# Kernel optimization log

Hardware: AMD Instinct MI355X
Metric: run time of the kernel (lower is better)

Reference implementation:

```python
import jax, jax.numpy as jnp
import numpy as np

B_, S_, IN_, D_, N_, K_ = 16, 4096, 64, 256, 16, 32


def _ln(x, g, b):
    m = jnp.mean(x, axis=-1, keepdims=True)
    v = jnp.var(x, axis=-1, keepdims=True)
    return (x - m) * jax.lax.rsqrt(v + 1e-5) * g + b


def setup_inputs() -> dict:
    key = jax.random.key(0)
    ks = jax.random.split(key, 24)
    s = 0.02
    d = dict(
        x=jax.random.normal(ks[0], (B_, S_, IN_), jnp.float32),
        W_in=jax.random.normal(ks[1], (IN_, D_)) * s, b_in=jnp.zeros((D_,)),
        ln1_g=jnp.ones((D_,)), ln1_b=jnp.zeros((D_,)),
        conv_w=jax.random.normal(ks[2], (D_, 1, 3)) * s, conv_b=jnp.zeros((D_,)),
        Wd=jax.random.normal(ks[3], (D_, D_)) * s, bd=jnp.zeros((D_,)),
        WB=jax.random.normal(ks[4], (D_, N_)) * s, bB=jnp.zeros((N_,)),
        WC=jax.random.normal(ks[5], (D_, N_)) * s, bC=jnp.zeros((N_,)),
        A=-jax.random.uniform(ks[6], (D_, N_)),
        Wg=jax.random.normal(ks[7], (D_, D_)) * s, bg=jnp.zeros((D_,)),
        filt_re=jax.random.normal(ks[8], (K_, D_)) * s,
        filt_im=jax.random.normal(ks[9], (K_, D_)) * s,
        alpha=jnp.ones((D_,)), beta=jnp.ones((D_,)),
        lnc_g=jnp.ones((D_,)), lnc_b=jnp.zeros((D_,)),
        W1=jax.random.normal(ks[10], (D_, D_ // 2)) * s, b1=jnp.zeros((D_ // 2,)),
        W2=jax.random.normal(ks[11], (D_ // 2, 2)) * s, b2=jnp.zeros((2,)),
    )
    return d


def reference(x, W_in, b_in, ln1_g, ln1_b, conv_w, conv_b, Wd, bd, WB, bB, WC, bC,
              A, Wg, bg, filt_re, filt_im, alpha, beta, lnc_g, lnc_b, W1, b1, W2, b2):
    xp = x @ W_in + b_in                                   # [B,S,D]

    # ---- TemporalBlock ----
    xn = _ln(xp, ln1_g, ln1_b)
    xc = jax.lax.conv_general_dilated(
        jnp.swapaxes(xn, 1, 2), conv_w, (1,), [(1, 1)],
        feature_group_count=D_, dimension_numbers=('NCH', 'OIH', 'NCH'))
    xc = jnp.swapaxes(xc + conv_b[:, None], 1, 2)          # [B,S,D]
    u = jax.nn.silu(xc)

    delta = jax.nn.softplus(u @ Wd + bd)                   # [B,S,D]
    Bm = u @ WB + bB                                       # [B,S,N]
    Cm = u @ WC + bC                                       # [B,S,N]

    def step(h, inp):
        u_t, d_t, B_t, C_t = inp                           # [B,D],[B,D],[B,N],[B,N]
        h = (1.0 + d_t[:, :, None] * A) * h + d_t[:, :, None] * B_t[:, None, :] * u_t[:, :, None]
        y_t = jnp.sum(C_t[:, None, :] * h, axis=-1)        # [B,D]
        return h, y_t

    h0 = jnp.zeros((u.shape[0], D_, N_), u.dtype)
    xs = tuple(jnp.swapaxes(a, 0, 1) for a in (u, delta, Bm, Cm))
    _, ys = jax.lax.scan(step, h0, xs)
    x_ssm = jnp.swapaxes(ys, 0, 1)                         # [B,S,D]
    g = jax.nn.silu(xn @ Wg + bg)
    x_t = xp + x_ssm * g

    # ---- SpectralBlock ----
    Xf = jnp.fft.rfft(xp, axis=1)                          # [B,F,D] complex
    mag = jnp.abs(Xf)
    _, idx = jax.lax.top_k(jnp.swapaxes(mag, 1, 2), K_)    # [B,D,K]
    idx = jnp.swapaxes(idx, 1, 2)                          # [B,K,D]
    sel = jnp.take_along_axis(Xf, idx, axis=1)             # [B,K,D]
    filt = filt_re + 1j * filt_im                          # [K,D]
    filtered = sel * filt[None]
    bi = jnp.arange(Xf.shape[0])[:, None, None]
    di = jnp.arange(D_)[None, None, :]
    Xfil = jnp.zeros_like(Xf).at[bi, idx, di].set(filtered)
    x_f = jnp.fft.irfft(Xfil, n=xp.shape[1], axis=1)       # [B,S,D]

    # ---- Fusion + classifier (eval: dropout = identity) ----
    z = alpha * x_t + beta * x_f
    zp = jnp.mean(z, axis=1)                               # [B,D]
    hcls = jax.nn.relu(_ln(zp, lnc_g, lnc_b) @ W1 + b1)
    return hcls @ W2 + b2                                  # [B,2]
```

## Files before the change

kernel.cpp:

```cpp
#include <hip/hip_runtime.h>
#include <hip/hip_bf16.h>
#include <math.h>

#define BB 16
#define SS 4096
#define IN 64
#define DD 256
#define NN 16
#define KK 32
#define CH 64
#define LCH 64
#define BS (BB*SS)

typedef __attribute__((ext_vector_type(4))) float f32x4;
typedef __attribute__((ext_vector_type(8))) short bf16x8;

__device__ __forceinline__ float bf2f(unsigned short u){
  return __uint_as_float(((unsigned int)u)<<16);
}
__device__ __forceinline__ unsigned short f2bf(float f){
  unsigned int u = __float_as_uint(f);
  return (unsigned short)((u + 0x7fffu + ((u>>16)&1u)) >> 16);
}
__device__ __forceinline__ float fast_softplus(float v){
  float e = __expf(-fabsf(v));
  return fmaxf(v, 0.f) + __logf(1.f + e);
}
__device__ __forceinline__ float fast_silu(float v){
  return v * __builtin_amdgcn_rcpf(1.f + __expf(-v));
}
__device__ __forceinline__ void* swz(void* base, int row, int byteoff){
  return (void*)((char*)base + (row<<9) + (byteoff ^ ((row&7)<<4)));
}
#define SW(i) ((i) ^ (((i)>>4)&15))
__device__ __forceinline__ int rev4(int k){
  return ((k&3)<<10) | (((k>>2)&3)<<8) | (((k>>4)&3)<<6)
       | (((k>>6)&3)<<4) | (((k>>8)&3)<<2) | ((k>>10)&3);
}

__global__ void k_prep(const float* Wd, const float* Wg, const float* WB, const float* WC,
                       const float* W_in, const float* bBv, const float* bCv,
                       unsigned short* WdF, unsigned short* WgF, unsigned short* WinF,
                       float* bbc, float2* tw){
  int id = blockIdx.x*256 + threadIdx.x;
  if (id < 73728){
    int jn = id >> 12; int rem = id & 4095;
    int kc = rem >> 9; int l8 = (rem >> 3) & 63; int e = id & 7;
    int lr = l8 & 15, lh = l8 >> 4;
    int k = kc*32 + lh*8 + e;
    float v;
    if (jn < 16){ int n = jn*16 + lr; v = Wd[k*256+n]; }
    else { int c = (jn-16)*16 + lr; v = (c<16) ? WB[k*16+c] : WC[k*16+(c-16)]; }
    WdF[id] = f2bf(v);
  }
  else if (id < 139264){
    int o = id - 73728;
    int jn = o >> 12; int rem = o & 4095;
    int kc = rem >> 9; int l8 = (rem >> 3) & 63; int e = o & 7;
    int lr = l8 & 15, lh = l8 >> 4;
    int k = kc*32 + lh*8 + e;
    WgF[o] = f2bf(Wg[k*256 + jn*16 + lr]);
  }
  else if (id < 155648){
    int o = id - 139264;
    int jn = o >> 10; int rem = o & 1023;
    int kc = rem >> 9; int l8 = (rem >> 3) & 63; int e = o & 7;
    int lr = l8 & 15, lh = l8 >> 4;
    int k = kc*32 + lh*8 + e;
    WinF[o] = f2bf(W_in[k*256 + jn*16 + lr]);
  }
  else if (id < 157696){ int k = id-155648;
    double a = -6.283185307179586476925287 * (double)k / 4096.0;
    tw[k] = make_float2((float)cos(a), (float)sin(a)); }
  else if (id < 157728){ int j = id-157696; bbc[j] = (j<16)? bBv[j] : bCv[j-16]; }
}

__global__ __launch_bounds__(256) void k_front(const float* x, const unsigned short* WinF, const float* b_in,
      const float* ln1_g, const float* ln1_b, const float* conv_w, const float* conv_b,
      float2* xpz, unsigned short* xn16, unsigned short* u16){
  __shared__ unsigned short xb[32*64];
  __shared__ float xs[20][260];
  int tid = threadIdx.x;
  int b = blockIdx.y; int t0 = blockIdx.x*16;
  {
    int row = tid>>3, slot = tid&7;
    int t = t0 - 1 + row;
    unsigned short h[8];
    if (row < 18 && t >= 0 && t < SS){
      const float* src = &x[((size_t)b*SS + t)*IN + slot*8];
      float4 v0 = *(const float4*)src;
      float4 v1 = *(const float4*)(src+4);
      h[0]=f2bf(v0.x); h[1]=f2bf(v0.y); h[2]=f2bf(v0.z); h[3]=f2bf(v0.w);
      h[4]=f2bf(v1.x); h[5]=f2bf(v1.y); h[6]=f2bf(v1.z); h[7]=f2bf(v1.w);
    } else {
      #pragma unroll
      for (int i=0;i<8;i++) h[i]=0;
    }
    *(uint4*)&xb[row*64 + ((slot ^ (row&7))<<3)] = *(uint4*)h;
  }
  __syncthreads();
  int wv = tid>>6, lane = tid&63, lr = lane&15, lh = lane>>4;
  {
    bf16x8 af[2][2];
    #pragma unroll
    for (int rf=0;rf<2;rf++)
      #pragma unroll
      for (int kc=0;kc<2;kc++){
        int row = rf*16 + lr;
        int slot = (kc*4 + lh) ^ (row&7);
        af[rf][kc] = *(const bf16x8*)&xb[row*64 + slot*8];
      }
    f32x4 acc[2][4];
    #pragma unroll
    for (int rf=0;rf<2;rf++)
      #pragma unroll
      for (int jj=0;jj<4;jj++){ acc[rf][jj][0]=0.f; acc[rf][jj][1]=0.f; acc[rf][jj][2]=0.f; acc[rf][jj][3]=0.f; }
    #pragma unroll
    for (int jj=0;jj<4;jj++){
      int jn = wv*4 + jj;
      const bf16x8* bp = (const bf16x8*)(WinF + (size_t)jn*1024 + (size_t)lane*8);
      bf16x8 b0 = bp[0];
      bf16x8 b1 = bp[64];
      #pragma unroll
      for (int rf=0;rf<2;rf++){
        acc[rf][jj] = __builtin_amdgcn_mfma_f32_16x16x32_bf16(af[rf][0], b0, acc[rf][jj], 0,0,0);
        acc[rf][jj] = __builtin_amdgcn_mfma_f32_16x16x32_bf16(af[rf][1], b1, acc[rf][jj], 0,0,0);
      }
    }
    #pragma unroll
    for (int jj=0;jj<4;jj++){
      int col = (wv*4+jj)*16 + lr;
      float bs = b_in[col];
      #pragma unroll
      for (int rf=0;rf<2;rf++){
        #pragma unroll
        for (int i=0;i<4;i++){
          int row = rf*16 + lh*4 + i;
          if (row < 18) xs[row][col] = acc[rf][jj][i] + bs;
        }
      }
    }
  }
  __syncthreads();
  {
    int sl = tid&15, p0 = tid>>4;
    float2* dst = xpz + (size_t)b*128*SS + t0 + sl;
    #pragma unroll
    for (int pass=0; pass<8; pass++){
      int p = p0 + 16*pass;
      float2 v = *(const float2*)&xs[1+sl][2*p];
      dst[(size_t)p*SS] = v;
    }
  }
  __syncthreads();
  float4 lg4 = *(const float4*)&ln1_g[lane*4];
  float4 lb4 = *(const float4*)&ln1_b[lane*4];
  for (int r=wv; r<18; r+=4){
    int t = t0 - 1 + r;
    bool valid = (t>=0) && (t<SS);
    float4 v = *(const float4*)&xs[r][lane*4];
    float s1 = v.x+v.y+v.z+v.w;
    float s2 = v.x*v.x+v.y*v.y+v.z*v.z+v.w*v.w;
    #pragma unroll
    for (int off=32; off; off>>=1){ s1 += __shfl_xor(s1,off); s2 += __shfl_xor(s2,off); }
    float mean = s1*(1.f/256.f);
    float var  = s2*(1.f/256.f) - mean*mean;
    float rstd = rsqrtf(var + 1e-5f);
    float o0 = valid ? ((v.x-mean)*rstd*lg4.x + lb4.x) : 0.f;
    float o1 = valid ? ((v.y-mean)*rstd*lg4.y + lb4.y) : 0.f;
    float o2 = valid ? ((v.z-mean)*rstd*lg4.z + lb4.z) : 0.f;
    float o3 = valid ? ((v.w-mean)*rstd*lg4.w + lb4.w) : 0.f;
    *(float4*)&xs[r][lane*4] = make_float4(o0,o1,o2,o3);
    if (r>=1 && r<=16){
      ushort4 st;
      st.x=f2bf(o0); st.y=f2bf(o1); st.z=f2bf(o2); st.w=f2bf(o3);
      *(ushort4*)&xn16[((size_t)b*SS + t)*DD + lane*4] = st;
    }
  }
  __syncthreads();
  int d = tid;
  float w0=conv_w[d*3], w1=conv_w[d*3+1], w2=conv_w[d*3+2], cb=conv_b[d];
  #pragma unroll 4
  for (int rr=0; rr<16; rr++){
    float a0=xs[rr][d], a1=xs[rr+1][d], a2=xs[rr+2][d];
    float xc = a0*w0 + a1*w1 + a2*w2 + cb;
    u16[((size_t)b*SS + (t0+rr))*DD + d] = f2bf(fast_silu(xc));
  }
}

template<int NTOT, int ACT>
__global__ __launch_bounds__(512,2) void k_gemm2(const unsigned short* Ab, const unsigned short* Bt,
      const float* bias_main, const float* bias_bc,
      unsigned int* out2, unsigned int* du2, unsigned short* out_bc){
  __shared__ unsigned short As[64*256];
  const int NF = NTOT/2;
  int tid = threadIdx.x;
  int m0 = blockIdx.x*64;
  {
    const uint4* gA = (const uint4*)(Ab + (size_t)m0*256);
    #pragma unroll
    for (int i=0;i<4;i++){
      int f = tid + 512*i;
      uint4 v = gA[f];
      *(uint4*)swz(As, f>>5, (f&31)<<4) = v;
    }
  }
  __syncthreads();
  int wv = tid>>6, lane = tid&63;
  int wm = wv>>1, nh = wv&1;
  int lr = lane&15, lh = lane>>4;
  const bf16x8* bbase = (const bf16x8*)(Bt + (size_t)(nh*NF)*4096 + (size_t)lane*8);
  f32x4 acc[NF];
  #pragma unroll
  for (int j=0;j<NF;j++){ acc[j][0]=0.f; acc[j][1]=0.f; acc[j][2]=0.f; acc[j][3]=0.f; }
  bf16x8 bq[2][8];
  #pragma unroll
  for (int kc=0;kc<8;kc++) bq[0][kc] = bbase[kc*64];
  #pragma unroll
  for (int j=0;j<NF;j++){
    if (j+1 < NF){
      #pragma unroll
      for (int kc=0;kc<8;kc++) bq[(j+1)&1][kc] = bbase[(j+1)*512 + kc*64];
    }
    #pragma unroll
    for (int kc=0;kc<8;kc++){
      bf16x8 af = *(const bf16x8*)swz(As, wm*16+lr, kc*64+lh*16);
      acc[j] = __builtin_amdgcn_mfma_f32_16x16x32_bf16(af, bq[j&1][kc], acc[j], 0,0,0);
    }
  }
  int row0 = m0 + wm*16 + lh*4;
  size_t pbase = ((size_t)row0 >> 1) * 256;
  #pragma unroll
  for (int j=0;j<NF;j++){
    int jn = nh*NF + j;
    if (jn < 16){
      int col = jn*16 + lr;
      float bs = bias_main[col];
      if (ACT==1){
        float de[4], du[4];
        #pragma unroll
        for (int i=0;i<4;i++){
          de[i] = fast_softplus(acc[j][i] + bs);
          float uu = bf2f(*(const unsigned short*)swz(As, wm*16+lh*4+i, col*2));
          du[i] = de[i]*uu;
        }
        out2[pbase + col]       = (unsigned int)f2bf(de[0]) | ((unsigned int)f2bf(de[1])<<16);
        out2[pbase + 256 + col] = (unsigned int)f2bf(de[2]) | ((unsigned int)f2bf(de[3])<<16);
        du2 [pbase + col]       = (unsigned int)f2bf(du[0]) | ((unsigned int)f2bf(du[1])<<16);
        du2 [pbase + 256 + col] = (unsigned int)f2bf(du[2]) | ((unsigned int)f2bf(du[3])<<16);
      } else {
        float g[4];
        #pragma unroll
        for (int i=0;i<4;i++) g[i] = fast_silu(acc[j][i] + bs);
        out2[pbase + col]       = (unsigned int)f2bf(g[0]) | ((unsigned int)f2bf(g[1])<<16);
        out2[pbase + 256 + col] = (unsigned int)f2bf(g[2]) | ((unsigned int)f2bf(g[3])<<16);
      }
    } else {
      int col = (jn-16)*16 + lr;
      float bs = bias_bc[col];
      #pragma unroll
      for (int i=0;i<4;i++){
        int row = m0 + wm*16 + lh*4 + i;
        out_bc[(size_t)row*32 + col] = f2bf(acc[j][i] + bs);
      }
    }
  }
}

__global__ __launch_bounds__(256,4) void k_fft(const float2* xpz, const float2* twg, int* rank, float* T0){
  __shared__ float2 buf[4096];
  __shared__ int scr8[8];
  int blk = blockIdx.x;
  int b = blk >> 7, pair = blk & 127;
  int tid = threadIdx.x;
  const float4* src4 = (const float4*)(xpz + ((size_t)b*128 + pair)*SS);
  #pragma unroll
  for (int q=tid; q<2048; q+=256){
    float4 v = src4[q];
    buf[SW(2*q)]   = make_float2(v.x, v.y);
    buf[SW(2*q+1)] = make_float2(v.z, v.w);
  }
  __syncthreads();
  int m = 1024, fac = 1;
  for (int st=0; st<6; st++){
    #pragma unroll
    for (int it=0; it<4; it++){
      int t = tid + 256*it;
      int j = t & (m-1);
      int i0 = 4*t - 3*j;
      float2 a0 = buf[SW(i0)];
      float2 a1 = buf[SW(i0+m)];
      float2 a2 = buf[SW(i0+2*m)];
      float2 a3 = buf[SW(i0+3*m)];
      float2 w1 = twg[j*fac];
      float2 w2 = make_float2(fmaf(w1.x,w1.x,-w1.y*w1.y), 2.f*w1.x*w1.y);
      float2 w3 = make_float2(fmaf(w1.x,w2.x,-w1.y*w2.y), fmaf(w1.x,w2.y, w1.y*w2.x));
      float t0x=a0.x+a2.x, t0y=a0.y+a2.y;
      float t1x=a0.x-a2.x, t1y=a0.y-a2.y;
      float t2x=a1.x+a3.x, t2y=a1.y+a3.y;
      float t3x=a1.y-a3.y, t3y=a3.x-a1.x;
      buf[SW(i0)]     = make_float2(t0x+t2x, t0y+t2y);
      float b1x = t1x+t3x, b1y = t1y+t3y;
      buf[SW(i0+m)]   = make_float2(fmaf(w1.x,b1x,-w1.y*b1y), fmaf(w1.x,b1y, w1.y*b1x));
      float b2x = t0x-t2x, b2y = t0y-t2y;
      buf[SW(i0+2*m)] = make_float2(fmaf(w2.x,b2x,-w2.y*b2y), fmaf(w2.x,b2y, w2.y*b2x));
      float b3x = t1x-t3x, b3y = t1y-t3y;
      buf[SW(i0+3*m)] = make_float2(fmaf(w3.x,b3x,-w3.y*b3y), fmaf(w3.x,b3y, w3.y*b3x));
    }
    __syncthreads();
    m >>= 2; fac <<= 2;
  }
  float2 z0 = buf[0];
  float thx = 4.f*z0.x*z0.x, thy = 4.f*z0.y*z0.y;
  int cx=0, cy=0;
  #pragma unroll
  for (int j=0;j<8;j++){
    int f = 1 + tid + 256*j;
    float2 zf = buf[SW(rev4(f))];
    float2 zc = buf[SW(rev4(4096-f))];
    float sxr = zf.x+zc.x, sxi = zf.y-zc.y;
    float syr = zf.x-zc.x, syi = zf.y+zc.y;
    cx += (fmaf(sxr,sxr,sxi*sxi) > thx) ? 1 : 0;
    cy += (fmaf(syr,syr,syi*syi) > thy) ? 1 : 0;
  }
  #pragma unroll
  for (int off=32; off; off>>=1){ cx += __shfl_xor(cx, off); cy += __shfl_xor(cy, off); }
  if ((tid&63)==0){ scr8[tid>>6] = cx; scr8[4+(tid>>6)] = cy; }
  __syncthreads();
  if (tid==0){
    int r0 = b*256 + 2*pair;
    rank[r0]   = scr8[0]+scr8[1]+scr8[2]+scr8[3];
    rank[r0+1] = scr8[4]+scr8[5]+scr8[6]+scr8[7];
    T0[r0]   = z0.x;
    T0[r0+1] = z0.y;
  }
}

__global__ __launch_bounds__(512) void k_scanA(const unsigned int* de2, const unsigned int* du2,
      const unsigned short* bc16, const float* Aw, float* AB_A, float* AB_B){
  __shared__ float bcs[LCH][16];
  int c = blockIdx.x, b = blockIdx.y;
  int t0 = c*LCH;
  int tid = threadIdx.x;
  {
    int t = tid>>3, q = tid&7;
    unsigned int v = *(const unsigned int*)(bc16 + ((size_t)b*SS + t0 + t)*32 + q*2);
    bcs[t][q*2]   = bf2f((unsigned short)(v & 0xffff));
    bcs[t][q*2+1] = bf2f((unsigned short)(v >> 16));
  }
  __syncthreads();
  int d = tid & 255, hf = tid >> 8;
  float aw[8];
  #pragma unroll
  for (int j=0;j<2;j++){
    float4 a4 = *(const float4*)&Aw[d*16 + hf*8 + j*4];
    aw[4*j]=a4.x; aw[4*j+1]=a4.y; aw[4*j+2]=a4.z; aw[4*j+3]=a4.w;
  }
  float Ac[8], Bc[8];
  #pragma unroll
  for (int n=0;n<8;n++){ Ac[n]=1.f; Bc[n]=0.f; }
  const unsigned int* DE = de2 + ((size_t)b*2048 + c*32)*256 + d;
  const unsigned int* DU = du2 + ((size_t)b*2048 + c*32)*256 + d;
  #pragma unroll 4
  for (int p=0;p<32;p++){
    unsigned int dv = DE[(size_t)p*256];
    unsigned int uv = DU[(size_t)p*256];
    float de0 = __uint_as_float(dv<<16);
    float de1 = __uint_as_float(dv&0xffff0000u);
    float du0 = __uint_as_float(uv<<16);
    float du1 = __uint_as_float(uv&0xffff0000u);
    {
      float4 B0 = *(const float4*)&bcs[2*p][hf*8];
      float4 B1 = *(const float4*)&bcs[2*p][hf*8+4];
      float bm[8] = {B0.x,B0.y,B0.z,B0.w, B1.x,B1.y,B1.z,B1.w};
      #pragma unroll
      for (int n=0;n<8;n++){
        float a = fmaf(de0, aw[n], 1.f);
        Ac[n] *= a;
        Bc[n] = fmaf(a, Bc[n], du0*bm[n]);
      }
    }
    {
      float4 B0 = *(const float4*)&bcs[2*p+1][hf*8];
      float4 B1 = *(const float4*)&bcs[2*p+1][hf*8+4];
      float bm[8] = {B0.x,B0.y,B0.z,B0.w, B1.x,B1.y,B1.z,B1.w};
      #pragma unroll
      for (int n=0;n<8;n++){
        float a = fmaf(de1, aw[n], 1.f);
        Ac[n] *= a;
        Bc[n] = fmaf(a, Bc[n], du1*bm[n]);
      }
    }
  }
  size_t o = (size_t)c*65536 + (size_t)b*4096 + (size_t)d*16 + hf*8;
  #pragma unroll
  for (int j=0;j<2;j++){
    *(float4*)&AB_A[o+4*j] = make_float4(Ac[4*j],Ac[4*j+1],Ac[4*j+2],Ac[4*j+3]);
    *(float4*)&AB_B[o+4*j] = make_float4(Bc[4*j],Bc[4*j+1],Bc[4*j+2],Bc[4*j+3]);
  }
}

__global__ void k_scanB(const float* AB_A, const float* AB_B, float* Hs){
  int tid = blockIdx.x*256 + threadIdx.x;
  float h = 0.f;
  #pragma unroll 8
  for (int c=0;c<CH;c++){
    Hs[c*65536 + tid] = h;
    h = fmaf(AB_A[c*65536 + tid], h, AB_B[c*65536 + tid]);
  }
}

__global__ __launch_bounds__(512) void k_scanC(const unsigned int* de2, const unsigned int* du2,
      const unsigned int* g2, const unsigned short* bc16, const float* Aw, const float* Hs, float* part){
  __shared__ float bcs[LCH][32];
  __shared__ float scr[256];
  int c = blockIdx.x, b = blockIdx.y;
  int t0 = c*LCH;
  int tid = threadIdx.x;
  {
    int t = tid>>3, q = tid&7;
    uint2 v = *(const uint2*)(bc16 + ((size_t)b*SS + t0 + t)*32 + q*4);
    bcs[t][q*4]   = bf2f((unsigned short)(v.x & 0xffff));
    bcs[t][q*4+1] = bf2f((unsigned short)(v.x >> 16));
    bcs[t][q*4+2] = bf2f((unsigned short)(v.y & 0xffff));
    bcs[t][q*4+3] = bf2f((unsigned short)(v.y >> 16));
  }
  __syncthreads();
  int d = tid & 255, hf = tid >> 8;
  float aw[8];
  #pragma unroll
  for (int j=0;j<2;j++){
    float4 a4 = *(const float4*)&Aw[d*16 + hf*8 + j*4];
    aw[4*j]=a4.x; aw[4*j+1]=a4.y; aw[4*j+2]=a4.z; aw[4*j+3]=a4.w;
  }
  float h[8];
  {
    size_t o = (size_t)c*65536 + (size_t)b*4096 + (size_t)d*16 + hf*8;
    #pragma unroll
    for (int j=0;j<2;j++){
      float4 h4 = *(const float4*)&Hs[o+4*j];
      h[4*j]=h4.x; h[4*j+1]=h4.y; h[4*j+2]=h4.z; h[4*j+3]=h4.w;
    }
  }
  float acc = 0.f;
  const unsigned int* DE = de2 + ((size_t)b*2048 + c*32)*256 + d;
  const unsigned int* DU = du2 + ((size_t)b*2048 + c*32)*256 + d;
  const unsigned int* G  = g2  + ((size_t)b*2048 + c*32)*256 + d;
  #pragma unroll 4
  for (int p=0;p<32;p++){
    unsigned int dv = DE[(size_t)p*256];
    unsigned int uv = DU[(size_t)p*256];
    unsigned int gv = G [(size_t)p*256];
    float de0 = __uint_as_float(dv<<16);
    float de1 = __uint_as_float(dv&0xffff0000u);
    float du0 = __uint_as_float(uv<<16);
    float du1 = __uint_as_float(uv&0xffff0000u);
    float gg0 = __uint_as_float(gv<<16);
    float gg1 = __uint_as_float(gv&0xffff0000u);
    {
      float4 B0 = *(const float4*)&bcs[2*p][hf*8];
      float4 B1 = *(const float4*)&bcs[2*p][hf*8+4];
      float4 C0 = *(const float4*)&bcs[2*p][16+hf*8];
      float4 C1 = *(const float4*)&bcs[2*p][16+hf*8+4];
      float bm[8] = {B0.x,B0.y,B0.z,B0.w, B1.x,B1.y,B1.z,B1.w};
      float cm[8] = {C0.x,C0.y,C0.z,C0.w, C1.x,C1.y,C1.z,C1.w};
      float y0 = 0.f, y1 = 0.f;
      #pragma unroll
      for (int n=0;n<8;n+=2){
        float a0 = fmaf(de0, aw[n],   1.f);
        float a1 = fmaf(de0, aw[n+1], 1.f);
        h[n]   = fmaf(a0, h[n],   du0*bm[n]);
        h[n+1] = fmaf(a1, h[n+1], du0*bm[n+1]);
        y0 = fmaf(cm[n],   h[n],   y0);
        y1 = fmaf(cm[n+1], h[n+1], y1);
      }
      acc = fmaf(y0+y1, gg0, acc);
    }
    {
      float4 B0 = *(const float4*)&bcs[2*p+1][hf*8];
      float4 B1 = *(const float4*)&bcs[2*p+1][hf*8+4];
      float4 C0 = *(const float4*)&bcs[2*p+1][16+hf*8];
      float4 C1 = *(const float4*)&bcs[2*p+1][16+hf*8+4];
      float bm[8] = {B0.x,B0.y,B0.z,B0.w, B1.x,B1.y,B1.z,B1.w};
      float cm[8] = {C0.x,C0.y,C0.z,C0.w, C1.x,C1.y,C1.z,C1.w};
      float y0 = 0.f, y1 = 0.f;
      #pragma unroll
      for (int n=0;n<8;n+=2){
        float a0 = fmaf(de1, aw[n],   1.f);
        float a1 = fmaf(de1, aw[n+1], 1.f);
        h[n]   = fmaf(a0, h[n],   du1*bm[n]);
        h[n+1] = fmaf(a1, h[n+1], du1*bm[n+1]);
        y0 = fmaf(cm[n],   h[n],   y0);
        y1 = fmaf(cm[n+1], h[n+1], y1);
      }
      acc = fmaf(y0+y1, gg1, acc);
    }
  }
  if (hf==1) scr[d] = acc;
  __syncthreads();
  if (hf==0) part[(size_t)(b*256 + d)*CH + c] = acc + scr[d];
}

__global__ __launch_bounds__(256) void k_final(const float* part, const float* T0, const int* rank,
      const float* alpha, const float* beta, const float* filt_re,
      const float* lnc_g, const float* lnc_b,
      const float* W1, const float* b1, const float* W2, const float* b2,
      float* out){
  __shared__ float zs[256];
  __shared__ float h1[128];
  __shared__ float red[8];
  int b = blockIdx.x, d = threadIdx.x;
  int row = b*256 + d;
  float ps = 0.f;
  #pragma unroll 8
  for (int c=0;c<CH;c++) ps += part[(size_t)row*CH + c];
  float ssm_mean = ps * (1.f/4096.f);
  float t0v = T0[row];
  float mxp = t0v * (1.f/4096.f);
  int r = rank[row];
  float spec = (r < KK) ? t0v * filt_re[r*DD + d] * (1.f/4096.f) : 0.f;
  float zp = alpha[d]*(mxp + ssm_mean) + beta[d]*spec;
  float s1 = zp, s2 = zp*zp;
  #pragma unroll
  for (int off=32; off; off>>=1){ s1 += __shfl_xor(s1,off); s2 += __shfl_xor(s2,off); }
  if ((d&63)==0){ red[d>>6] = s1; red[4+(d>>6)] = s2; }
  __syncthreads();
  float mean = (red[0]+red[1]+red[2]+red[3]) * (1.f/256.f);
  float var  = (red[4]+red[5]+red[6]+red[7]) * (1.f/256.f) - mean*mean;
  float ln = (zp-mean)*rsqrtf(var+1e-5f)*lnc_g[d] + lnc_b[d];
  zs[d] = ln;
  __syncthreads();
  if (d < 128){
    float acc = b1[d];
    #pragma unroll 16
    for (int k=0;k<256;k++) acc = fmaf(zs[k], W1[k*128+d], acc);
    h1[d] = fmaxf(acc, 0.f);
  }
  __syncthreads();
  if (d < 2){
    float acc = b2[d];
    #pragma unroll 16
    for (int k=0;k<128;k++) acc = fmaf(h1[k], W2[k*2+d], acc);
    out[b*2+d] = acc;
  }
}

extern "C" void kernel_launch(void* const* d_in, const int* in_sizes, int n_in,
                              void* d_out, int out_size, void* d_ws, size_t ws_size,
                              hipStream_t stream){
  const float* x      = (const float*)d_in[0];
  const float* W_in   = (const float*)d_in[1];
  const float* b_in   = (const float*)d_in[2];
  const float* ln1_g  = (const float*)d_in[3];
  const float* ln1_b  = (const float*)d_in[4];
  const float* conv_w = (const float*)d_in[5];
  const float* conv_b = (const float*)d_in[6];
  const float* Wd     = (const float*)d_in[7];
  const float* bd     = (const float*)d_in[8];
  const float* WB     = (const float*)d_in[9];
  const float* bB     = (const float*)d_in[10];
  const float* WC     = (const float*)d_in[11];
  const float* bC     = (const float*)d_in[12];
  const float* A      = (const float*)d_in[13];
  const float* Wg     = (const float*)d_in[14];
  const float* bg     = (const float*)d_in[15];
  const float* filt_re= (const float*)d_in[16];
  const float* alpha  = (const float*)d_in[18];
  const float* beta   = (const float*)d_in[19];
  const float* lnc_g  = (const float*)d_in[20];
  const float* lnc_b  = (const float*)d_in[21];
  const float* W1     = (const float*)d_in[22];
  const float* b1     = (const float*)d_in[23];
  const float* W2     = (const float*)d_in[24];
  const float* b2     = (const float*)d_in[25];

  char* w = (char*)d_ws;
  unsigned int* de2 = (unsigned int*)(w);
  unsigned int* du2 = (unsigned int*)(w + 33554432);
  float2* xpz = (float2*)(w + 67108864);
  float* AB_A = (float*)(w + 67108864);
  float* AB_B = (float*)(w + 67108864 + 16777216);
  float* Hs   = (float*)(w + 67108864 + 33554432);
  unsigned short* bc16 = (unsigned short*)(w + 67108864 + 50331648);
  float* part = (float*)(w + 67108864 + 54525952);
  unsigned short* xn16 = (unsigned short*)(w + 134217728);
  unsigned short* u16  = (unsigned short*)(w + 167772160);
  unsigned int* g2 = (unsigned int*)(w + 201326592);
  char* small = w + 234881024;
  unsigned short* WdF  = (unsigned short*)(small);
  unsigned short* WgF  = (unsigned short*)(small + 147456);
  unsigned short* WinF = (unsigned short*)(small + 278528);
  float*  bbc = (float*)(small + 311296);
  float2* tw  = (float2*)(small + 311424);
  float*  T0  = (float*)(small + 327808);
  int*    rank= (int*)(small + 344192);
  (void)in_sizes; (void)n_in; (void)out_size; (void)ws_size;

  hipLaunchKernelGGL(k_prep, dim3(617), dim3(256), 0, stream,
                     Wd, Wg, WB, WC, W_in, bB, bC, WdF, WgF, WinF, bbc, tw);
  hipLaunchKernelGGL(k_front, dim3(SS/16, BB), dim3(256), 0, stream,
                     x, WinF, b_in, ln1_g, ln1_b, conv_w, conv_b, xpz, xn16, u16);
  hipLaunchKernelGGL(k_fft, dim3(BB*128), dim3(256), 0, stream, xpz, tw, rank, T0);
  hipLaunchKernelGGL((k_gemm2<18,1>), dim3(BS/64), dim3(512), 0, stream,
                     u16, WdF, bd, bbc, de2, du2, bc16);
  hipLaunchKernelGGL((k_gemm2<16,2>), dim3(BS/64), dim3(512), 0, stream,
                     xn16, WgF, bg, bbc, g2, (unsigned int*)nullptr, bc16);
  hipLaunchKernelGGL(k_scanA, dim3(CH, BB), dim3(512), 0, stream, de2, du2, bc16, A, AB_A, AB_B);
  hipLaunchKernelGGL(k_scanB, dim3(256), dim3(256), 0, stream, AB_A, AB_B, Hs);
  hipLaunchKernelGGL(k_scanC, dim3(CH, BB), dim3(512), 0, stream, de2, du2, g2, bc16, A, Hs, part);
  hipLaunchKernelGGL(k_final, dim3(BB), dim3(256), 0, stream,
                     part, T0, rank, alpha, beta, filt_re, lnc_g, lnc_b, W1, b1, W2, b2, (float*)d_out);
}
```

Baseline: 236.5 us.

## Fuse Wd/WB/WC and Wg GEMMs into front kernel via shared-memory tiles

Moves the delta/B/C projection and gate projection GEMMs into k_front. The normalized activations and conv+silu outputs now stay in shared memory instead of going out to global bf16 buffers and back. Two kernel launches and the global round-trip of xn16/u16 are removed. In exchange each 256-thread block does 16-row GEMMs that re-read the full weight matrices from global/L2 per block, with more LDS use and lower MFMA reuse.

New measurement: 254.7 us. 1.08x slower.

```diff
diff --git a/kernel.cpp b/kernel.cpp
--- a/kernel.cpp
+++ b/kernel.cpp
@@ -75,11 +75,16 @@
   else if (id < 157728){ int j = id-157696; bbc[j] = (j<16)? bBv[j] : bCv[j-16]; }
 }
 
-__global__ __launch_bounds__(256) void k_front(const float* x, const unsigned short* WinF, const float* b_in,
+__global__ __launch_bounds__(256) void k_front(const float* x, const unsigned short* WinF,
+      const unsigned short* WdF, const unsigned short* WgF, const float* b_in,
       const float* ln1_g, const float* ln1_b, const float* conv_w, const float* conv_b,
-      float2* xpz, unsigned short* xn16, unsigned short* u16){
+      const float* bd, const float* bg, const float* bbc,
+      float2* xpz, unsigned int* de2, unsigned int* du2, unsigned int* g2,
+      unsigned short* out_bc){
   __shared__ unsigned short xb[32*64];
   __shared__ float xs[20][260];
+  __shared__ unsigned short us[16*256];
+  __shared__ unsigned short xns[16*256];
   int tid = threadIdx.x;
   int b = blockIdx.y; int t0 = blockIdx.x*16;
   {
@@ -174,94 +179,77 @@
     if (r>=1 && r<=16){
       ushort4 st;
       st.x=f2bf(o0); st.y=f2bf(o1); st.z=f2bf(o2); st.w=f2bf(o3);
-      *(ushort4*)&xn16[((size_t)b*SS + t)*DD + lane*4] = st;
-    }
-  }
-  __syncthreads();
-  int d = tid;
-  float w0=conv_w[d*3], w1=conv_w[d*3+1], w2=conv_w[d*3+2], cb=conv_b[d];
-  #pragma unroll 4
-  for (int rr=0; rr<16; rr++){
-    float a0=xs[rr][d], a1=xs[rr+1][d], a2=xs[rr+2][d];
-    float xc = a0*w0 + a1*w1 + a2*w2 + cb;
-    u16[((size_t)b*SS + (t0+rr))*DD + d] = f2bf(fast_silu(xc));
-  }
-}
-
-template<int NTOT, int ACT>
-__global__ __launch_bounds__(512,2) void k_gemm2(const unsigned short* Ab, const unsigned short* Bt,
-      const float* bias_main, const float* bias_bc,
-      unsigned int* out2, unsigned int* du2, unsigned short* out_bc){
-  __shared__ unsigned short As[64*256];
-  const int NF = NTOT/2;
-  int tid = threadIdx.x;
-  int m0 = blockIdx.x*64;
-  {
-    const uint4* gA = (const uint4*)(Ab + (size_t)m0*256);
-    #pragma unroll
-    for (int i=0;i<4;i++){
-      int f = tid + 512*i;
-      uint4 v = gA[f];
-      *(uint4*)swz(As, f>>5, (f&31)<<4) = v;
-    }
-  }
-  __syncthreads();
-  int wv = tid>>6, lane = tid&63;
-  int wm = wv>>1, nh = wv&1;
-  int lr = lane&15, lh = lane>>4;
-  const bf16x8* bbase = (const bf16x8*)(Bt + (size_t)(nh*NF)*4096 + (size_t)lane*8);
-  f32x4 acc[NF];
-  #pragma unroll
-  for (int j=0;j<NF;j++){ acc[j][0]=0.f; acc[j][1]=0.f; acc[j][2]=0.f; acc[j][3]=0.f; }
-  bf16x8 bq[2][8];
-  #pragma unroll
-  for (int kc=0;kc<8;kc++) bq[0][kc] = bbase[kc*64];
-  #pragma unroll
-  for (int j=0;j<NF;j++){
-    if (j+1 < NF){
-      #pragma unroll
-      for (int kc=0;kc<8;kc++) bq[(j+1)&1][kc] = bbase[(j+1)*512 + kc*64];
-    }
-    #pragma unroll
-    for (int kc=0;kc<8;kc++){
-      bf16x8 af = *(const bf16x8*)swz(As, wm*16+lr, kc*64+lh*16);
-      acc[j] = __builtin_amdgcn_mfma_f32_16x16x32_bf16(af, bq[j&1][kc], acc[j], 0,0,0);
-    }
-  }
-  int row0 = m0 + wm*16 + lh*4;
-  size_t pbase = ((size_t)row0 >> 1) * 256;
-  #pragma unroll
-  for (int j=0;j<NF;j++){
-    int jn = nh*NF + j;
-    if (jn < 16){
-      int col = jn*16 + lr;
-      float bs = bias_main[col];
-      if (ACT==1){
-        float de[4], du[4];
-        #pragma unroll
-        for (int i=0;i<4;i++){
-          de[i] = fast_softplus(acc[j][i] + bs);
-          float uu = bf2f(*(const unsigned short*)swz(As, wm*16+lh*4+i, col*2));
-          du[i] = de[i]*uu;
+      *(ushort4*)swz(xns, r-1, lane*8) = st;
+    }
+  }
+  __syncthreads();
+  {
+    int d = tid;
+    float w0=conv_w[d*3], w1=conv_w[d*3+1], w2=conv_w[d*3+2], cb=conv_b[d];
+    #pragma unroll 4
+    for (int rr=0; rr<16; rr++){
+      float a0=xs[rr][d], a1=xs[rr+1][d], a2=xs[rr+2][d];
+      float xc = a0*w0 + a1*w1 + a2*w2 + cb;
+      *(unsigned short*)swz(us, rr, d*2) = f2bf(fast_silu(xc));
+    }
+  }
+  __syncthreads();
+  {
+    bool isWd = (wv < 2);
+    const unsigned short* Atile = isWd ? us : xns;
+    const unsigned short* Bw    = isWd ? WdF : WgF;
+    int jn0   = isWd ? (wv*9)     : ((wv-2)*8);
+    int njn   = isWd ? 9 : 8;
+    bf16x8 af[8];
+    #pragma unroll
+    for (int kc=0;kc<8;kc++)
+      af[kc] = *(const bf16x8*)swz((void*)Atile, lr, kc*64+lh*16);
+    int row0 = t0 + lh*4;
+    size_t pbase = ((size_t)b*4096 + row0) >> 1;
+    pbase *= 256;
+    for (int jj=0; jj<njn; jj++){
+      int jn = jn0 + jj;
+      const bf16x8* bp = (const bf16x8*)(Bw + (size_t)jn*4096 + (size_t)lane*8);
+      bf16x8 bq[8];
+      #pragma unroll
+      for (int kc=0;kc<8;kc++) bq[kc] = bp[kc*64];
+      f32x4 acc;
+      acc[0]=0.f; acc[1]=0.f; acc[2]=0.f; acc[3]=0.f;
+      #pragma unroll
+      for (int kc=0;kc<8;kc++)
+        acc = __builtin_amdgcn_mfma_f32_16x16x32_bf16(af[kc], bq[kc], acc, 0,0,0);
+      if (isWd){
+        if (jn < 16){
+          int col = jn*16 + lr;
+          float bs = bd[col];
+          float de[4], du[4];
+          #pragma unroll
+          for (int i=0;i<4;i++){
+            de[i] = fast_softplus(acc[i] + bs);
+            float uu = bf2f(*(const unsigned short*)swz((void*)us, lh*4+i, col*2));
+            du[i] = de[i]*uu;
+          }
+          de2[pbase + col]       = (unsigned int)f2bf(de[0]) | ((unsigned int)f2bf(de[1])<<16);
+          de2[pbase + 256 + col] = (unsigned int)f2bf(de[2]) | ((unsigned int)f2bf(de[3])<<16);
+          du2[pbase + col]       = (unsigned int)f2bf(du[0]) | ((unsigned int)f2bf(du[1])<<16);
+          du2[pbase + 256 + col] = (unsigned int)f2bf(du[2]) | ((unsigned int)f2bf(du[3])<<16);
+        } else {
+          int col = (jn-16)*16 + lr;
+          float bs = bbc[col];
+          #pragma unroll
+          for (int i=0;i<4;i++){
+            int row = t0 + lh*4 + i;
+            out_bc[((size_t)b*SS + row)*32 + col] = f2bf(acc[i] + bs);
+          }
         }
-        out2[pbase + col]       = (unsigned int)f2bf(de[0]) | ((unsigned int)f2bf(de[1])<<16);
-        out2[pbase + 256 + col] = (unsigned int)f2bf(de[2]) | ((unsigned int)f2bf(de[3])<<16);
-        du2 [pbase + col]       = (unsigned int)f2bf(du[0]) | ((unsigned int)f2bf(du[1])<<16);
-        du2 [pbase + 256 + col] = (unsigned int)f2bf(du[2]) | ((unsigned int)f2bf(du[3])<<16);
       } else {
+        int col = jn*16 + lr;
+        float bs = bg[col];
         float g[4];
         #pragma unroll
-        for (int i=0;i<4;i++) g[i] = fast_silu(acc[j][i] + bs);
-        out2[pbase + col]       = (unsigned int)f2bf(g[0]) | ((unsigned int)f2bf(g[1])<<16);
-        out2[pbase + 256 + col] = (unsigned int)f2bf(g[2]) | ((unsigned int)f2bf(g[3])<<16);
-      }
-    } else {
-      int col = (jn-16)*16 + lr;
-      float bs = bias_bc[col];
-      #pragma unroll
-      for (int i=0;i<4;i++){
-        int row = m0 + wm*16 + lh*4 + i;
-        out_bc[(size_t)row*32 + col] = f2bf(acc[j][i] + bs);
+        for (int i=0;i<4;i++) g[i] = fast_silu(acc[i] + bs);
+        g2[pbase + col]       = (unsigned int)f2bf(g[0]) | ((unsigned int)f2bf(g[1])<<16);
+        g2[pbase + 256 + col] = (unsigned int)f2bf(g[2]) | ((unsigned int)f2bf(g[3])<<16);
       }
     }
   }
@@ -581,10 +569,8 @@
   float* AB_A = (float*)(w + 67108864);
   float* AB_B = (float*)(w + 67108864 + 16777216);
   float* Hs   = (float*)(w + 67108864 + 33554432);
-  unsigned short* bc16 = (unsigned short*)(w + 67108864 + 50331648);
-  float* part = (float*)(w + 67108864 + 54525952);
-  unsigned short* xn16 = (unsigned short*)(w + 134217728);
-  unsigned short* u16  = (unsigned short*)(w + 167772160);
+  float* part = (float*)(w + 67108864 + 50331648);
+  unsigned short* bc16 = (unsigned short*)(w + 134217728);
   unsigned int* g2 = (unsigned int*)(w + 201326592);
   char* small = w + 234881024;
   unsigned short* WdF  = (unsigned short*)(small);
@@ -599,12 +585,9 @@
   hipLaunchKernelGGL(k_prep, dim3(617), dim3(256), 0, stream,
                      Wd, Wg, WB, WC, W_in, bB, bC, WdF, WgF, WinF, bbc, tw);
   hipLaunchKernelGGL(k_front, dim3(SS/16, BB), dim3(256), 0, stream,
-                     x, WinF, b_in, ln1_g, ln1_b, conv_w, conv_b, xpz, xn16, u16);
+                     x, WinF, WdF, WgF, b_in, ln1_g, ln1_b, conv_w, conv_b,
+                     bd, bg, bbc, xpz, de2, du2, g2, bc16);
   hipLaunchKernelGGL(k_fft, dim3(BB*128), dim3(256), 0, stream, xpz, tw, rank, T0);
-  hipLaunchKernelGGL((k_gemm2<18,1>), dim3(BS/64), dim3(512), 0, stream,
-                     u16, WdF, bd, bbc, de2, du2, bc16);
-  hipLaunchKernelGGL((k_gemm2<16,2>), dim3(BS/64), dim3(512), 0, stream,
-                     xn16, WgF, bg, bbc, g2, (unsigned int*)nullptr, bc16);
   hipLaunchKernelGGL(k_scanA, dim3(CH, BB), dim3(512), 0, stream, de2, du2, bc16, A, AB_A, AB_B);
   hipLaunchKernelGGL(k_scanB, dim3(256), dim3(256), 0, stream, AB_A, AB_B, Hs);
   hipLaunchKernelGGL(k_scanC, dim3(CH, BB), dim3(512), 0, stream, de2, du2, g2, bc16, A, Hs, part);
```
